# Performance work log

Measured on AMD Instinct MI355X. Metric: run time of the kernel, lower is better.

## Reference

```python
import jax, jax.numpy as jnp
import numpy as np
from jax import lax

B, T, D_IN, H, L = 8, 256, 6, 200, 200


def setup_inputs() -> dict:
    key = jax.random.key(0)
    ks = jax.random.split(key, 12)
    s = 0.05  # small init to avoid gate saturation across 200 layers
    return {
        "x":    jax.random.normal(ks[0], (B, T, D_IN), dtype=jnp.float32),
        "W1":   jax.random.normal(ks[1], (H, D_IN), dtype=jnp.float32) * s,
        "b1":   jnp.zeros((H,), dtype=jnp.float32),
        "Wih":  jax.random.normal(ks[2], (L, 4 * H, H), dtype=jnp.float32) * s,
        "Whh":  jax.random.normal(ks[3], (L, 4 * H, H), dtype=jnp.float32) * s,
        "bih":  jnp.zeros((L, 4 * H), dtype=jnp.float32),
        "bhh":  jnp.zeros((L, 4 * H), dtype=jnp.float32),
        "W2a":  jax.random.normal(ks[4], (50, H), dtype=jnp.float32) * s,
        "b2a":  jnp.zeros((50,), dtype=jnp.float32),
        "W2b":  jax.random.normal(ks[5], (24, 50), dtype=jnp.float32) * s,
        "b2b":  jnp.zeros((24,), dtype=jnp.float32),
    }


def _lstm_stack(seq, Wih, Whh, bih, bhh):
    # seq: [B, T, H]; stacked weights over L layers.
    def layer_step(carry_seq, params):
        wih, whh, bi, bh = params  # [4H,H], [4H,H], [4H], [4H]
        xs = jnp.swapaxes(carry_seq, 0, 1)  # [T, B, H]

        def cell(hc, xt):
            h, c = hc
            gates = xt @ wih.T + bi + h @ whh.T + bh  # [B, 4H]
            i, f, g, o = jnp.split(gates, 4, axis=-1)  # PyTorch ifgo order
            c = jax.nn.sigmoid(f) * c + jax.nn.sigmoid(i) * jnp.tanh(g)
            h = jax.nn.sigmoid(o) * jnp.tanh(c)
            return (h, c), h

        h0 = jnp.zeros((carry_seq.shape[0], H), dtype=carry_seq.dtype)
        _, ys = lax.scan(cell, (h0, h0), xs)
        return jnp.swapaxes(ys, 0, 1), None  # [B, T, H]

    out, _ = lax.scan(layer_step, seq, (Wih, Whh, bih, bhh))
    return out


def reference(x, W1, b1, Wih, Whh, bih, bhh, W2a, b2a, W2b, b2b):
    h = x @ W1.T + b1                      # mlp1: [B,T,200]
    h = _lstm_stack(h, Wih, Whh, bih, bhh)  # 200-layer stacked LSTM
    h = jax.nn.relu(h @ W2a.T + b2a)       # mlp2 hidden
    return h @ W2b.T + b2b                 # [B,T,24]
```

## Files before the change

### kernel.cpp

```cpp
#include <hip/hip_runtime.h>
#include <hip/hip_bf16.h>
#include <stdint.h>

#define B 8
#define T 256
#define DIN 6
#define H 200
#define G 800
#define L 200

#define NT 13
#define KT 13
#define NFRAG 169
#define F_RG 117
#define F_LD 52
#define XPAD 424

#define SENT16 0xFFFFu
#define SENT64 0xFFFFFFFFFFFFFFFFull

#define OFF_H0    8192
#define OFF_FINAL (OFF_H0 + (B*T*H)/2)
#define OFF_RING  (OFF_FINAL + B*T*H)
#define CFLAG(l)  (4096 + (l) * 16)

typedef _Float16 half8 __attribute__((ext_vector_type(8)));
typedef float f32x4 __attribute__((ext_vector_type(4)));
typedef unsigned long long u64t;

__device__ __forceinline__ float fsig(float x) {
    return 1.0f / (1.0f + __expf(-x));
}
__device__ __forceinline__ float ftanh(float x) {
    float e = __expf(2.0f * x);
    return 1.0f - 2.0f / (e + 1.0f);
}

__device__ __forceinline__ uint32_t ld_flag(const uint32_t* p) {
    return __hip_atomic_load(p, __ATOMIC_RELAXED, __HIP_MEMORY_SCOPE_AGENT);
}
__device__ __forceinline__ void st_flag(uint32_t* p, uint32_t v) {
    __hip_atomic_store(p, v, __ATOMIC_RELAXED, __HIP_MEMORY_SCOPE_AGENT);
}
__device__ __forceinline__ u64t ld_u64(const u64t* p) {
    return __hip_atomic_load(p, __ATOMIC_RELAXED, __HIP_MEMORY_SCOPE_AGENT);
}
__device__ __forceinline__ void st_u64(u64t* p, u64t v) {
    __hip_atomic_store(p, v, __ATOMIC_RELAXED, __HIP_MEMORY_SCOPE_AGENT);
}
__device__ __forceinline__ uint8_t to_fp8(float v) {
    return (uint8_t)(__builtin_amdgcn_cvt_pk_fp8_f32(v, v, 0u, false) & 0xffu);
}

__global__ void init_flags(uint32_t* ws) {
    int i = blockIdx.x * 256 + threadIdx.x;
    if (i < 8192) ws[i] = 0u;
}

__global__ void fill_ring(u64t* __restrict__ ring, long n) {
    long i = (long)blockIdx.x * 256 + threadIdx.x;
    if (i < n) ring[i] = SENT64;
}

__global__ void mlp1_kernel(const float* __restrict__ x, const float* __restrict__ W1,
                            const float* __restrict__ b1, uint16_t* __restrict__ h0h) {
    int idx = blockIdx.x * 256 + threadIdx.x;
    if (idx >= B * T * H) return;
    int j  = idx % H;
    int bt = idx / H;
    int b  = bt / T;
    int t  = bt % T;
    const float* xr = x  + (size_t)bt * DIN;
    const float* wr = W1 + (size_t)j * DIN;
    float a = b1[j];
#pragma unroll
    for (int k = 0; k < DIN; ++k) a += xr[k] * wr[k];
    _Float16 h = (_Float16)a;
    h0h[((size_t)(t * 2 + (b >> 2)) * H + j) * 4 + (b & 3)] = __builtin_bit_cast(uint16_t, h);
}

__global__ void convert_weights_mfma(const float* __restrict__ Wih,
                                     const float* __restrict__ Whh,
                                     u64t* __restrict__ Wm8) {
    size_t idx = (size_t)blockIdx.x * 256 + threadIdx.x;
    const size_t TOT = (size_t)L * 4 * NFRAG * 64;
    if (idx >= TOT) return;
    int lane = (int)(idx & 63);
    size_t r0 = idx >> 6;
    int f = (int)(r0 % NFRAG); r0 /= NFRAG;
    int g = (int)(r0 % 4);
    int l = (int)(r0 / 4);
    int kt = f / 13, nt = f % 13;
    int rl = nt * 16 + (lane & 15);
    int r  = g * 200 + rl;
    float v[8];
#pragma unroll
    for (int j = 0; j < 8; ++j) {
        int k = kt * 32 + (lane >> 4) * 8 + j;
        float xx = 0.0f;
        if (rl < 200 && k < 400)
            xx = (k < 200) ? Wih[((size_t)l * G + r) * 200 + k]
                           : Whh[((size_t)l * G + r) * 200 + (k - 200)];
        v[j] = xx;
    }
    uint32_t lo = __builtin_amdgcn_cvt_pk_fp8_f32(v[0], v[1], 0u, false);
    lo = __builtin_amdgcn_cvt_pk_fp8_f32(v[2], v[3], lo, true);
    uint32_t hi = __builtin_amdgcn_cvt_pk_fp8_f32(v[4], v[5], 0u, false);
    hi = __builtin_amdgcn_cvt_pk_fp8_f32(v[6], v[7], hi, true);
    Wm8[((size_t)(l * 4 + g) * NFRAG + f) * 64 + lane] = (u64t)lo | ((u64t)hi << 32);
}

#define MFMA8(a, b, c)  __builtin_amdgcn_mfma_f32_16x16x32_fp8_fp8((a), (b), (c), 0, 0, 0)
#define LDA8(kt) (*(const long*)&xh8[(lane & 15) * XPAD + (kt) * 32 + (lane >> 4) * 8])

template <int NTB, int NTN>
__device__ __forceinline__ void run_fast(
    int l, int tid, int g, int lane, int R,
    const u64t* __restrict__ wq8,
    u64t* wl8, uint8_t* xh8, float* zl,
    const u64t* __restrict__ h0h, u64t* ring, float* finalbuf, uint32_t* flags,
    const float* __restrict__ bih, const float* __restrict__ bhh)
{
#pragma clang fp contract(fast)
    const int rmask = R - 1;
    const int word  = tid / 200;
    const int j     = tid - word * 200;
    const bool act  = tid < 400;

    float cs[4];
    float bs[4];
    if (act) {
#pragma unroll
        for (int gg = 0; gg < 4; ++gg)
            bs[gg] = bih[(size_t)l * G + gg * H + j] + bhh[(size_t)l * G + gg * H + j];
#pragma unroll
        for (int b = 0; b < 4; ++b) cs[b] = 0.0f;
    }

    u64t wr[9 * NTN];
#pragma unroll
    for (int kt = 0; kt < 9; ++kt)
#pragma unroll
        for (int n = 0; n < NTN; ++n)
            wr[kt * NTN + n] = wq8[(kt * 13 + NTB + n) * 64 + lane];
    if (NTB == 0) {
        for (int i = 0; i < F_LD; ++i)
            wl8[(g * F_LD + i) * 64 + lane] = wq8[(F_RG + i) * 64 + lane];
    }
    __syncthreads();

    for (int t = 0; t < T; ++t) {
        f32x4 acc[NTN];
#pragma unroll
        for (int n = 0; n < NTN; ++n) acc[n] = (f32x4){0.f, 0.f, 0.f, 0.f};

#pragma unroll
        for (int kt = 7; kt < 9; ++kt) {
            long a = LDA8(kt);
#pragma unroll
            for (int n = 0; n < NTN; ++n)
                acc[n] = MFMA8(a, (long)wr[kt * NTN + n], acc[n]);
        }
#pragma unroll
        for (int kt = 9; kt < 13; ++kt) {
            long a = LDA8(kt);
#pragma unroll
            for (int n = 0; n < NTN; ++n) {
                u64t w = wl8[(g * F_LD + (kt - 9) * 13 + NTB + n) * 64 + lane];
                acc[n] = MFMA8(a, (long)w, acc[n]);
            }
        }

        if (l < L - 1 && t >= R) {
            const uint32_t need = (uint32_t)(t - R + 1);
            while (ld_flag(&flags[CFLAG(l + 1)]) < need) __builtin_amdgcn_s_sleep(1);
        }

        if (act) {
            u64t p;
            if (l == 0) {
                p = h0h[(size_t)t * 400 + tid];
            } else {
                u64t* s = ring + ((size_t)(l - 1) * R + (t & rmask)) * 400 + tid;
                p = ld_u64(s);
                while ((uint16_t)(p >> 48) == SENT16) {
                    __builtin_amdgcn_s_sleep(1);
                    p = ld_u64(s);
                }
                st_u64(s, SENT64);
            }
#pragma unroll
            for (int bb = 0; bb < 4; ++bb) {
                float f = (float)__builtin_bit_cast(_Float16, (uint16_t)(p >> (16 * bb)));
                xh8[(word * 4 + bb) * XPAD + j] = to_fp8(f);
            }
        }
        __syncthreads();

#pragma unroll
        for (int kt = 0; kt < 7; ++kt) {
            long a = LDA8(kt);
#pragma unroll
            for (int n = 0; n < NTN; ++n)
                acc[n] = MFMA8(a, (long)wr[kt * NTN + n], acc[n]);
        }

        if ((lane >> 4) < 2) {
#pragma unroll
            for (int n = 0; n < NTN; ++n) {
                int nj = (NTB + n) * 16 + (lane & 15);
#pragma unroll
                for (int r = 0; r < 4; ++r) {
                    int b = (lane >> 4) * 4 + r;
                    zl[(g * 8 + b) * 208 + nj] = acc[n][r];
                }
            }
        }
        asm volatile("s_waitcnt vmcnt(0)" ::: "memory");
        __syncthreads();
        if (tid == 0 && l > 0) st_flag(&flags[CFLAG(l)], (uint32_t)(t + 1));

        if (act) {
            u64t p = 0ull;
#pragma unroll
            for (int bb = 0; bb < 4; ++bb) {
                int b = word * 4 + bb;
                float zi = zl[(0 * 8 + b) * 208 + j] + bs[0];
                float zf = zl[(1 * 8 + b) * 208 + j] + bs[1];
                float zg = zl[(2 * 8 + b) * 208 + j] + bs[2];
                float zo = zl[(3 * 8 + b) * 208 + j] + bs[3];
                float ig = fsig(zi);
                float fg = fsig(zf);
                float gg = ftanh(zg);
                float og = fsig(zo);
                float c  = fg * cs[bb] + ig * gg;
                cs[bb] = c;
                float h = og * ftanh(c);
                xh8[b * XPAD + 200 + j] = to_fp8(h);
                _Float16 hh = (_Float16)h;
                p |= (u64t)__builtin_bit_cast(uint16_t, hh) << (16 * bb);
                if (l == L - 1) finalbuf[((size_t)b * T + t) * H + j] = h;
            }
            if (l < L - 1) {
                st_u64(ring + ((size_t)l * R + (t & rmask)) * 400 + tid, p);
            }
        }
        __syncthreads();
    }
}

template <bool FAST>
__global__ __launch_bounds__(512, 2)
void lstm_pipeline(const u64t* __restrict__ Wm8,
                   const float* __restrict__ Wih, const float* __restrict__ Whh,
                   const float* __restrict__ bih, const float* __restrict__ bhh,
                   float* ws, int R) {
#pragma clang fp contract(fast)
    const int bx    = blockIdx.x;
    const int l     = ((bx & 7) * 25) + (bx >> 3);
    const int tid   = threadIdx.x;
    const int wv    = tid >> 6;
    const int g     = wv & 3;
    const int half  = wv >> 2;
    const int lane  = tid & 63;
    const int rmask = R - 1;

    const u64t* h0h = (const u64t*)(ws + OFF_H0);
    float*    finalbuf = ws + OFF_FINAL;
    u64t*     ring     = (u64t*)(ws + OFF_RING);
    uint32_t* flags    = (uint32_t*)ws;

    __shared__ __align__(16) uint8_t  xh8[16 * XPAD];
    __shared__ __align__(16) float    zl[4 * 8 * 208];
    __shared__ __align__(16) u64t     wl8[4 * F_LD * 64];

    for (int i = tid; i < (16 * XPAD) / 16; i += 512)
        ((uint4*)xh8)[i] = make_uint4(0u, 0u, 0u, 0u);

    if (FAST) {
        const u64t* wq8 = Wm8 + (size_t)(l * 4 + g) * NFRAG * 64;
        if (half == 0)
            run_fast<0, 7>(l, tid, g, lane, R, wq8, wl8, xh8, zl,
                           h0h, ring, finalbuf, flags, bih, bhh);
        else
            run_fast<7, 6>(l, tid, g, lane, R, wq8, wl8, xh8, zl,
                           h0h, ring, finalbuf, flags, bih, bhh);
        return;
    }

    float* xhf = (float*)wl8;
    const bool actj = tid < H;
    float cs[B];
    float bs[4];
    if (actj) {
#pragma unroll
        for (int gg = 0; gg < 4; ++gg)
            bs[gg] = bih[(size_t)l * G + gg * H + tid] + bhh[(size_t)l * G + gg * H + tid];
#pragma unroll
        for (int b = 0; b < B; ++b) cs[b] = 0.0f;
    }
    __syncthreads();

    for (int t = 0; t < T; ++t) {
        if (l < L - 1 && t >= R) {
            const uint32_t need = (uint32_t)(t - R + 1);
            while (ld_flag(&flags[CFLAG(l + 1)]) < need) __builtin_amdgcn_s_sleep(1);
        }
        if (actj) {
            u64t p0, p1;
            if (l == 0) {
                p0 = h0h[(size_t)t * 400 + tid];
                p1 = h0h[(size_t)t * 400 + 200 + tid];
            } else {
                u64t* s = ring + ((size_t)(l - 1) * R + (t & rmask)) * 400;
                p0 = ld_u64(s + tid);
                p1 = ld_u64(s + 200 + tid);
                while ((uint16_t)(p0 >> 48) == SENT16 ||
                       (uint16_t)(p1 >> 48) == SENT16) {
                    __builtin_amdgcn_s_sleep(1);
                    p0 = ld_u64(s + tid);
                    p1 = ld_u64(s + 200 + tid);
                }
                st_u64(s + tid, SENT64);
                st_u64(s + 200 + tid, SENT64);
            }
#pragma unroll
            for (int b = 0; b < 4; ++b) {
                xhf[b * 416 + tid]       = (float)__builtin_bit_cast(_Float16, (uint16_t)(p0 >> (16 * b)));
                xhf[(b + 4) * 416 + tid] = (float)__builtin_bit_cast(_Float16, (uint16_t)(p1 >> (16 * b)));
            }
        }
        asm volatile("s_waitcnt vmcnt(0)" ::: "memory");
        __syncthreads();
        if (tid == 0 && l > 0) st_flag(&flags[CFLAG(l)], (uint32_t)(t + 1));

        if (actj) {
            const float* wi0 = Wih + (size_t)l * G * H;
            const float* wh0 = Whh + (size_t)l * G * H;
            float acc[4][B];
#pragma unroll
            for (int gg = 0; gg < 4; ++gg)
#pragma unroll
                for (int b = 0; b < B; ++b) acc[gg][b] = 0.0f;
            for (int k2 = 0; k2 < 200; ++k2) {
                float2 wvv[4];
                if (k2 < 100) {
#pragma unroll
                    for (int gg = 0; gg < 4; ++gg)
                        wvv[gg] = *(const float2*)&wi0[((size_t)(gg * 200 + tid)) * 200 + 2 * k2];
                } else {
#pragma unroll
                    for (int gg = 0; gg < 4; ++gg)
                        wvv[gg] = *(const float2*)&wh0[((size_t)(gg * 200 + tid)) * 200 + 2 * (k2 - 100)];
                }
#pragma unroll
                for (int b = 0; b < B; ++b) {
                    float2 xv = *(const float2*)&xhf[b * 416 + 2 * k2];
#pragma unroll
                    for (int gg = 0; gg < 4; ++gg) {
                        acc[gg][b] += wvv[gg].x * xv.x;
                        acc[gg][b] += wvv[gg].y * xv.y;
                    }
                }
            }
#pragma unroll
            for (int gg = 0; gg < 4; ++gg)
#pragma unroll
                for (int b = 0; b < B; ++b)
                    zl[(gg * 8 + b) * 208 + tid] = acc[gg][b];
        }
        __syncthreads();

        if (actj) {
            u64t p0 = 0ull, p1 = 0ull;
#pragma unroll
            for (int b = 0; b < B; ++b) {
                float zi = zl[(0 * 8 + b) * 208 + tid] + bs[0];
                float zf = zl[(1 * 8 + b) * 208 + tid] + bs[1];
                float zg = zl[(2 * 8 + b) * 208 + tid] + bs[2];
                float zo = zl[(3 * 8 + b) * 208 + tid] + bs[3];
                float ig = fsig(zi);
                float fg = fsig(zf);
                float gg = ftanh(zg);
                float og = fsig(zo);
                float c  = fg * cs[b] + ig * gg;
                cs[b] = c;
                float h = og * ftanh(c);
                xhf[b * 416 + 200 + tid] = h;
                _Float16 hh = (_Float16)h;
                u64t u = (u64t)__builtin_bit_cast(uint16_t, hh);
                if (b < 4) p0 |= u << (16 * b);
                else       p1 |= u << (16 * (b - 4));
                if (l == L - 1) finalbuf[((size_t)b * T + t) * H + tid] = h;
            }
            if (l < L - 1) {
                u64t* dst = ring + ((size_t)l * R + (t & rmask)) * 400;
                st_u64(dst + tid, p0);
                st_u64(dst + 200 + tid, p1);
            }
        }
        __syncthreads();
    }
}

__global__ __launch_bounds__(64)
void mlp2_kernel(const float* __restrict__ fin, const float* __restrict__ W2a,
                 const float* __restrict__ b2a, const float* __restrict__ W2b,
                 const float* __restrict__ b2b, float* __restrict__ out) {
    const int bt  = blockIdx.x;
    const int tid = threadIdx.x;
    __shared__ float sx[H];
    __shared__ float sh[50];
    for (int i = tid; i < H; i += 64) sx[i] = fin[(size_t)bt * H + i];
    __syncthreads();
    if (tid < 50) {
        float a = b2a[tid];
        const float* w = W2a + (size_t)tid * H;
        for (int k = 0; k < H; ++k) a += w[k] * sx[k];
        sh[tid] = fmaxf(a, 0.0f);
    }
    __syncthreads();
    if (tid < 24) {
        float a = b2b[tid];
        const float* w = W2b + (size_t)tid * 50;
#pragma unroll
        for (int m = 0; m < 50; ++m) a += w[m] * sh[m];
        out[(size_t)bt * 24 + tid] = a;
    }
}

extern "C" void kernel_launch(void* const* d_in, const int* in_sizes, int n_in,
                              void* d_out, int out_size, void* d_ws, size_t ws_size,
                              hipStream_t stream) {
    const float* x    = (const float*)d_in[0];
    const float* W1   = (const float*)d_in[1];
    const float* b1   = (const float*)d_in[2];
    const float* Wih  = (const float*)d_in[3];
    const float* Whh  = (const float*)d_in[4];
    const float* bihp = (const float*)d_in[5];
    const float* bhhp = (const float*)d_in[6];
    const float* W2a  = (const float*)d_in[7];
    const float* b2a  = (const float*)d_in[8];
    const float* W2b  = (const float*)d_in[9];
    const float* b2b  = (const float*)d_in[10];
    float* out = (float*)d_out;
    float* ws  = (float*)d_ws;

    const size_t wm8_u32 = (size_t)L * 4 * NFRAG * 64 * 2;
    const size_t ring_u32_per_R = (size_t)(L - 1) * B * H / 2;

    int R = 8; bool fast = false; size_t offwm = 0;
    for (;;) {
        size_t o = (OFF_RING + (size_t)R * ring_u32_per_R + 3) & ~(size_t)3;
        if ((o + wm8_u32) * 4ull <= ws_size) { fast = true; offwm = o; break; }
        if (R == 1) break;
        R >>= 1;
    }
    if (!fast) {
        R = 8;
        while (R > 1 && (OFF_RING + (size_t)R * ring_u32_per_R) * 4ull > ws_size)
            R >>= 1;
    }
    u64t* Wm8 = (u64t*)(ws + offwm);

    const long ring_u64 = (long)(L - 1) * R * 400;

    init_flags<<<32, 256, 0, stream>>>((uint32_t*)d_ws);
    fill_ring<<<(int)((ring_u64 + 255) / 256), 256, 0, stream>>>(
        (u64t*)(ws + OFF_RING), ring_u64);
    mlp1_kernel<<<(B * T * H + 255) / 256, 256, 0, stream>>>(x, W1, b1,
                                                             (uint16_t*)(ws + OFF_H0));
    if (fast) {
        const size_t conv_threads = (size_t)L * 4 * NFRAG * 64;
        convert_weights_mfma<<<(int)((conv_threads + 255) / 256), 256, 0, stream>>>(
            Wih, Whh, Wm8);
        lstm_pipeline<true><<<L, 512, 0, stream>>>(Wm8, Wih, Whh, bihp, bhhp, ws, R);
    } else {
        lstm_pipeline<false><<<L, 512, 0, stream>>>(Wm8, Wih, Whh, bihp, bhhp, ws, R);
    }
    mlp2_kernel<<<B * T, 64, 0, stream>>>(ws + OFF_FINAL, W2a, b2a, W2b, b2b, out);
}
```

Baseline: 2.113 ms.

## Split LSTM layer block into 16 waves, prefetch ring input, batch flag publishing

Each layer block now runs 1024 threads instead of 512. The 13 gate N-tiles are split across four wave groups (4/3/3/3 tiles) instead of two, which shrinks the per-wave register-resident weight fragments and spreads the LDS weight staging across all groups. The next timestep's input from the inter-layer ring (or from h0) is prefetched one step ahead, so the global load latency is hidden behind the current step's MFMAs. The consumer-progress flag is now published only every 4 steps, and the last-seen flag value is cached locally to reduce polling and vmcnt drains. The trade-offs are more barrier participants per step, possible register pressure from the 1024-thread launch bound, and producers being held back longer by the coarser flag updates.

```diff
diff --git a/kernel.cpp b/kernel.cpp
--- a/kernel.cpp
+++ b/kernel.cpp
@@ -115,7 +115,7 @@
 
 template <int NTB, int NTN>
 __device__ __forceinline__ void run_fast(
-    int l, int tid, int g, int lane, int R,
+    int l, int tid, int g, int q, int lane, int R,
     const u64t* __restrict__ wq8,
     u64t* wl8, uint8_t* xh8, float* zl,
     const u64t* __restrict__ h0h, u64t* ring, float* finalbuf, uint32_t* flags,
@@ -143,10 +143,15 @@
 #pragma unroll
         for (int n = 0; n < NTN; ++n)
             wr[kt * NTN + n] = wq8[(kt * 13 + NTB + n) * 64 + lane];
-    if (NTB == 0) {
-        for (int i = 0; i < F_LD; ++i)
-            wl8[(g * F_LD + i) * 64 + lane] = wq8[(F_RG + i) * 64 + lane];
-    }
+    for (int i = q * 13; i < q * 13 + 13; ++i)
+        wl8[(g * F_LD + i) * 64 + lane] = wq8[(F_RG + i) * 64 + lane];
+
+    u64t pf = SENT64;
+    if (act) {
+        if (l == 0) pf = h0h[tid];
+        else        pf = ld_u64(ring + ((size_t)(l - 1) * R) * 400 + tid);
+    }
+    uint32_t cfl = 0;
     __syncthreads();
 
     for (int t = 0; t < T; ++t) {
@@ -173,19 +178,22 @@
 
         if (l < L - 1 && t >= R) {
             const uint32_t need = (uint32_t)(t - R + 1);
-            while (ld_flag(&flags[CFLAG(l + 1)]) < need) __builtin_amdgcn_s_sleep(1);
+            while (cfl < need) {
+                cfl = ld_flag(&flags[CFLAG(l + 1)]);
+                if (cfl >= need) break;
+                __builtin_amdgcn_s_sleep(1);
+            }
         }
 
         if (act) {
-            u64t p;
-            if (l == 0) {
-                p = h0h[(size_t)t * 400 + tid];
-            } else {
+            u64t p = pf;
+            if (l > 0) {
                 u64t* s = ring + ((size_t)(l - 1) * R + (t & rmask)) * 400 + tid;
-                p = ld_u64(s);
-                while ((uint16_t)(p >> 48) == SENT16) {
-                    __builtin_amdgcn_s_sleep(1);
-                    p = ld_u64(s);
+                if ((uint16_t)(p >> 48) == SENT16) {
+                    do {
+                        __builtin_amdgcn_s_sleep(1);
+                        p = ld_u64(s);
+                    } while ((uint16_t)(p >> 48) == SENT16);
                 }
                 st_u64(s, SENT64);
             }
@@ -194,6 +202,9 @@
                 float f = (float)__builtin_bit_cast(_Float16, (uint16_t)(p >> (16 * bb)));
                 xh8[(word * 4 + bb) * XPAD + j] = to_fp8(f);
             }
+            int tn = (t + 1 < T) ? t + 1 : t;
+            if (l == 0) pf = h0h[(size_t)tn * 400 + tid];
+            else        pf = ld_u64(ring + ((size_t)(l - 1) * R + (tn & rmask)) * 400 + tid);
         }
         __syncthreads();
 
@@ -216,9 +227,10 @@
                 }
             }
         }
-        asm volatile("s_waitcnt vmcnt(0)" ::: "memory");
-        __syncthreads();
-        if (tid == 0 && l > 0) st_flag(&flags[CFLAG(l)], (uint32_t)(t + 1));
+        const bool pub = ((t & 3) == 3) || (t == T - 1);
+        if (pub) asm volatile("s_waitcnt vmcnt(0)" ::: "memory");
+        __syncthreads();
+        if (pub && tid == 0 && l > 0) st_flag(&flags[CFLAG(l)], (uint32_t)(t + 1));
 
         if (act) {
             u64t p = 0ull;
@@ -250,7 +262,7 @@
 }
 
 template <bool FAST>
-__global__ __launch_bounds__(512, 2)
+__global__ __launch_bounds__(1024, 4)
 void lstm_pipeline(const u64t* __restrict__ Wm8,
                    const float* __restrict__ Wih, const float* __restrict__ Whh,
                    const float* __restrict__ bih, const float* __restrict__ bhh,
@@ -261,7 +273,7 @@
     const int tid   = threadIdx.x;
     const int wv    = tid >> 6;
     const int g     = wv & 3;
-    const int half  = wv >> 2;
+    const int q     = wv >> 2;
     const int lane  = tid & 63;
     const int rmask = R - 1;
 
@@ -274,17 +286,21 @@
     __shared__ __align__(16) float    zl[4 * 8 * 208];
     __shared__ __align__(16) u64t     wl8[4 * F_LD * 64];
 
-    for (int i = tid; i < (16 * XPAD) / 16; i += 512)
+    for (int i = tid; i < (16 * XPAD) / 16; i += 1024)
         ((uint4*)xh8)[i] = make_uint4(0u, 0u, 0u, 0u);
 
     if (FAST) {
         const u64t* wq8 = Wm8 + (size_t)(l * 4 + g) * NFRAG * 64;
-        if (half == 0)
-            run_fast<0, 7>(l, tid, g, lane, R, wq8, wl8, xh8, zl,
-                           h0h, ring, finalbuf, flags, bih, bhh);
-        else
-            run_fast<7, 6>(l, tid, g, lane, R, wq8, wl8, xh8, zl,
-                           h0h, ring, finalbuf, flags, bih, bhh);
+        switch (q) {
+        case 0:  run_fast<0, 4>(l, tid, g, q, lane, R, wq8, wl8, xh8, zl,
+                                h0h, ring, finalbuf, flags, bih, bhh); break;
+        case 1:  run_fast<4, 3>(l, tid, g, q, lane, R, wq8, wl8, xh8, zl,
+                                h0h, ring, finalbuf, flags, bih, bhh); break;
+        case 2:  run_fast<7, 3>(l, tid, g, q, lane, R, wq8, wl8, xh8, zl,
+                                h0h, ring, finalbuf, flags, bih, bhh); break;
+        default: run_fast<10, 3>(l, tid, g, q, lane, R, wq8, wl8, xh8, zl,
+                                 h0h, ring, finalbuf, flags, bih, bhh); break;
+        }
         return;
     }
 
@@ -474,9 +490,9 @@
         const size_t conv_threads = (size_t)L * 4 * NFRAG * 64;
         convert_weights_mfma<<<(int)((conv_threads + 255) / 256), 256, 0, stream>>>(
             Wih, Whh, Wm8);
-        lstm_pipeline<true><<<L, 512, 0, stream>>>(Wm8, Wih, Whh, bihp, bhhp, ws, R);
+        lstm_pipeline<true><<<L, 1024, 0, stream>>>(Wm8, Wih, Whh, bihp, bhhp, ws, R);
     } else {
-        lstm_pipeline<false><<<L, 512, 0, stream>>>(Wm8, Wih, Whh, bihp, bhhp, ws, R);
+        lstm_pipeline<false><<<L, 1024, 0, stream>>>(Wm8, Wih, Whh, bihp, bhhp, ws, R);
     }
     mlp2_kernel<<<B * T, 64, 0, stream>>>(ws + OFF_FINAL, W2a, b2a, W2b, b2b, out);
 }
```

Result: no change. 2.149 ms (+1.7%).
